# Kernel tuning notes

Hardware: AMD Instinct MI355X
Metric: run time of the kernel (lower is better)

## Reference

```python
import jax, jax.numpy as jnp
import numpy as np
from jax import lax

B, C, H, W = 2, 384, 32, 32
N_HEAD, N_GROUP = 12, 6
HC = C // N_HEAD          # 32 head channels
GC = C // N_GROUP         # 64 group channels
GH = N_HEAD // N_GROUP    # 2 heads per group
KK = 7                    # depthwise kernel (25<=32<=48)
OFF_FACTOR = 2.0
SCALE = HC ** -0.5
EPS = 1e-5


def setup_inputs() -> dict:
    key = jax.random.key(0)
    ks = jax.random.split(key, 16)
    s = 0.02
    inp = {
        "x": jax.random.normal(ks[0], (B, C, H, W), jnp.float32),
        "Wq": jax.random.normal(ks[1], (C, C), jnp.float32) * s,
        "bq": jnp.zeros((C,), jnp.float32),
        "Wk": jax.random.normal(ks[2], (C, C), jnp.float32) * s,
        "bk": jnp.zeros((C,), jnp.float32),
        "Wv": jax.random.normal(ks[3], (C, C), jnp.float32) * s,
        "bv": jnp.zeros((C,), jnp.float32),
        "Wo": jax.random.normal(ks[4], (C, C), jnp.float32) * s,
        "bo": jnp.zeros((C,), jnp.float32),
        "off_dw_w": jax.random.normal(ks[5], (GC, 1, KK, KK), jnp.float32) * s,  # depthwise OIHW
        "off_dw_b": jnp.zeros((GC,), jnp.float32),
        "ln_g": jnp.ones((GC,), jnp.float32),
        "ln_b": jnp.zeros((GC,), jnp.float32),
        "off_pw_w": jax.random.normal(ks[6], (2, GC), jnp.float32) * s,  # 1x1 conv, no bias
        "rpe_table": jax.random.normal(ks[7], (N_HEAD, 2 * H - 1, 2 * W - 1), jnp.float32) * 0.01,
    }
    return inp


def _ref_points(Hk, Wk):
    # torch.linspace(0.5, Hk-0.5, Hk)/Hk*2-1 == ((i+0.5)/Hk)*2-1
    ry = ((jnp.arange(Hk, dtype=jnp.float32) + 0.5) / Hk) * 2.0 - 1.0
    rx = ((jnp.arange(Wk, dtype=jnp.float32) + 0.5) / Wk) * 2.0 - 1.0
    gy, gx = jnp.meshgrid(ry, rx, indexing='ij')
    return jnp.stack((gy, gx), axis=-1)  # [Hk, Wk, 2] in (y, x) order


def _grid_sample(img, grid):
    # img: [N, Cc, Hi, Wi]; grid: [N, Hg, Wg, 2] in (x, y), align_corners=True, zeros padding
    N, Cc, Hi, Wi = img.shape
    Hg, Wg = grid.shape[1], grid.shape[2]
    gx = (grid[..., 0] + 1.0) * 0.5 * (Wi - 1)
    gy = (grid[..., 1] + 1.0) * 0.5 * (Hi - 1)
    x0 = jnp.floor(gx)
    y0 = jnp.floor(gy)
    wx = gx - x0
    wy = gy - y0
    img_f = img.reshape(N, Cc, Hi * Wi)

    def corner(xi, yi, w):
        valid = (xi >= 0) & (xi <= Wi - 1) & (yi >= 0) & (yi <= Hi - 1)
        xc = jnp.clip(xi, 0, Wi - 1).astype(jnp.int32)
        yc = jnp.clip(yi, 0, Hi - 1).astype(jnp.int32)
        idx = (yc * Wi + xc).reshape(N, 1, Hg * Wg)
        vals = jnp.take_along_axis(img_f, jnp.broadcast_to(idx, (N, Cc, Hg * Wg)), axis=2)
        w = (w * valid.astype(img.dtype)).reshape(N, 1, Hg * Wg)
        return vals * w

    out = (corner(x0, y0, (1 - wx) * (1 - wy))
           + corner(x0 + 1, y0, wx * (1 - wy))
           + corner(x0, y0 + 1, (1 - wx) * wy)
           + corner(x0 + 1, y0 + 1, wx * wy))
    return out.reshape(N, Cc, Hg, Wg)


def _conv1x1(x, w, b=None):
    y = jnp.einsum('bchw,oc->bohw', x, w)
    if b is not None:
        y = y + b[None, :, None, None]
    return y


def _forward(x, Wq, bq, Wk, bk, Wv, bv, Wo, bo, off_dw_w, off_dw_b, ln_g, ln_b, off_pw_w, rpe_table):
    q = _conv1x1(x, Wq, bq)                                        # [B, C, H, W]
    q_off = q.reshape(B * N_GROUP, GC, H, W)
    # conv_offset: depthwise conv -> LayerNorm(ch) -> GELU -> 1x1 conv to 2 ch
    o = lax.conv_general_dilated(q_off, off_dw_w, (1, 1), ((KK // 2, KK // 2), (KK // 2, KK // 2)),
                                 feature_group_count=GC,
                                 dimension_numbers=('NCHW', 'OIHW', 'NCHW'))
    o = o + off_dw_b[None, :, None, None]
    mu = jnp.mean(o, axis=1, keepdims=True)
    var = jnp.mean((o - mu) ** 2, axis=1, keepdims=True)
    o = (o - mu) * lax.rsqrt(var + EPS) * ln_g[None, :, None, None] + ln_b[None, :, None, None]
    o = jax.nn.gelu(o, approximate=False)
    off = jnp.einsum('bchw,oc->bohw', o, off_pw_w)                 # [BG, 2, Hs, Ws]
    Hs, Ws = off.shape[2], off.shape[3]
    n_sample = Hs * Ws
    off_range = jnp.array([1.0 / Hs, 1.0 / Ws], jnp.float32).reshape(1, 2, 1, 1)
    off = jnp.tanh(off) * off_range * OFF_FACTOR
    off = jnp.transpose(off, (0, 2, 3, 1))                         # [BG, Hs, Ws, 2] (y, x)
    pos = off + _ref_points(Hs, Ws)[None]                          # [BG, Hs, Ws, 2]

    x_g = x.reshape(B * N_GROUP, GC, H, W)
    x_s = _grid_sample(x_g, pos[..., ::-1])                        # [BG, GC, Hs, Ws]
    x_s = x_s.reshape(B, C, 1, n_sample)

    k = _conv1x1(x_s, Wk, bk).reshape(B * N_HEAD, HC, n_sample)
    v = _conv1x1(x_s, Wv, bv).reshape(B * N_HEAD, HC, n_sample)
    qh = q.reshape(B * N_HEAD, HC, H * W)
    attn = jnp.einsum('bcm,bcn->bmn', qh, k) * SCALE               # [BH, HW, ns]

    # RPE: bilinear lookup of relative-position table at query-sample displacements
    q_grid = _ref_points(H, W).reshape(1, H * W, 1, 2)
    disp = (q_grid - pos.reshape(B * N_GROUP, 1, n_sample, 2)) * 0.5  # [BG, HW, ns, 2] (y, x)
    rpe_b = jnp.broadcast_to(rpe_table[None], (B, N_HEAD, 2 * H - 1, 2 * W - 1))
    rpe_b = rpe_b.reshape(B * N_GROUP, GH, 2 * H - 1, 2 * W - 1)
    attn_bias = _grid_sample(rpe_b, disp[..., ::-1])               # [BG, GH, HW, ns]
    attn = attn + attn_bias.reshape(B * N_HEAD, H * W, n_sample)

    attn = jax.nn.softmax(attn, axis=2)
    out = jnp.einsum('bmn,bcn->bcm', attn, v).reshape(B, C, H, W)
    y = _conv1x1(out, Wo, bo)
    return y


def reference(x, Wq, bq, Wk, bk, Wv, bv, Wo, bo, off_dw_w, off_dw_b, ln_g, ln_b, off_pw_w, rpe_table):
    return _forward(x, Wq, bq, Wk, bk, Wv, bv, Wo, bo,
                    off_dw_w, off_dw_b, ln_g, ln_b, off_pw_w, rpe_table)
```

## Files before the change

### kernel.cpp

```cpp
#include <hip/hip_runtime.h>
#include <hip/hip_fp16.h>
#include <math.h>

#define HH 32
#define WW 32
#define HWSZ 1024
#define CC 384
#define NHEAD 12
#define NGROUP 6
#define HC 32
#define GC 64
#define NS 1024
#define ATTN_SCALE 0.17677669529663687f

typedef _Float16 half8_t __attribute__((ext_vector_type(8)));
typedef _Float16 half4_t __attribute__((ext_vector_type(4)));
typedef _Float16 half2_t __attribute__((ext_vector_type(2)));
typedef float    f4_t    __attribute__((ext_vector_type(4)));

template<int XLO>
__global__ __launch_bounds__(256) void gemm_wx(
    const float* __restrict__ W, const float* __restrict__ bias,
    const float* __restrict__ X, float* __restrict__ Y)
{
    const int bz = blockIdx.z;
    const int tm = blockIdx.y * 32;
    const int tn = blockIdx.x * 64;
    const int tid = threadIdx.x;
    const int w = tid >> 6, lane = tid & 63;
    const int quad = lane >> 4, lcol = lane & 15;

    __shared__ _Float16 sWh[32][40];
    __shared__ _Float16 sXh[64][40];
    __shared__ _Float16 sXl[XLO ? 64 : 1][40];

    const float* Xb = X + (size_t)bz * CC * 1024;
    float* Yb = Y + (size_t)bz * CC * 1024;

    f4_t acc0 = {0.f, 0.f, 0.f, 0.f}, acc1 = {0.f, 0.f, 0.f, 0.f};

    for (int k0 = 0; k0 < CC; k0 += 32) {
        {
            int m = tid >> 3, k4 = (tid & 7) * 4;
            float4 wv = *(const float4*)&W[(size_t)(tm + m) * CC + k0 + k4];
            half4_t h; h[0] = (_Float16)wv.x; h[1] = (_Float16)wv.y;
            h[2] = (_Float16)wv.z; h[3] = (_Float16)wv.w;
            *(half4_t*)&sWh[m][k4] = h;
        }
        {
            int k = tid >> 3, nj = tid & 7;
            const float* xr = &Xb[(size_t)(k0 + k) * 1024 + tn + nj];
#pragma unroll
            for (int i = 0; i < 8; ++i) {
                float v = xr[8 * i];
                _Float16 h = (_Float16)v;
                sXh[nj + 8 * i][k] = h;
                if (XLO) sXl[nj + 8 * i][k] = (_Float16)(v - (float)h);
            }
        }
        __syncthreads();

        half8_t Ah0 = *(const half8_t*)&sWh[lcol][quad * 8];
        half8_t Ah1 = *(const half8_t*)&sWh[16 + lcol][quad * 8];
        half8_t Bh  = *(const half8_t*)&sXh[w * 16 + lcol][quad * 8];
        acc0 = __builtin_amdgcn_mfma_f32_16x16x32_f16(Ah0, Bh, acc0, 0, 0, 0);
        acc1 = __builtin_amdgcn_mfma_f32_16x16x32_f16(Ah1, Bh, acc1, 0, 0, 0);
        if (XLO) {
            half8_t Bl = *(const half8_t*)&sXl[w * 16 + lcol][quad * 8];
            acc0 = __builtin_amdgcn_mfma_f32_16x16x32_f16(Ah0, Bl, acc0, 0, 0, 0);
            acc1 = __builtin_amdgcn_mfma_f32_16x16x32_f16(Ah1, Bl, acc1, 0, 0, 0);
        }
        __syncthreads();
    }

#pragma unroll
    for (int r = 0; r < 4; ++r) {
        int m0 = tm + quad * 4 + r;
        Yb[(size_t)m0 * 1024 + tn + w * 16 + lcol]        = acc0[r] + bias[m0];
        Yb[(size_t)(m0 + 16) * 1024 + tn + w * 16 + lcol] = acc1[r] + bias[m0 + 16];
    }
}

__global__ __launch_bounds__(256) void gemm_kv_fused(
    const float* __restrict__ Wk, const float* __restrict__ bk,
    const float* __restrict__ Wv, const float* __restrict__ bv,
    const float* __restrict__ X,
    _Float16* __restrict__ khT, _Float16* __restrict__ vhb)
{
    const int bz = blockIdx.z;
    const int head = blockIdx.y;
    const int tm = head * 32;
    const int tn = blockIdx.x * 64;
    const int tid = threadIdx.x;
    const int w = tid >> 6, lane = tid & 63;
    const int quad = lane >> 4, lcol = lane & 15;
    const int bh = bz * 12 + head;

    __shared__ _Float16 sWk[32][40], sWv[32][40];
    __shared__ _Float16 sXh[64][40];

    const float* Xb = X + (size_t)bz * CC * 1024;

    f4_t ak0 = {0.f, 0.f, 0.f, 0.f}, ak1 = {0.f, 0.f, 0.f, 0.f};
    f4_t av0 = {0.f, 0.f, 0.f, 0.f}, av1 = {0.f, 0.f, 0.f, 0.f};

    for (int k0 = 0; k0 < CC; k0 += 32) {
        {
            int m = tid >> 3, k4 = (tid & 7) * 4;
            float4 wk = *(const float4*)&Wk[(size_t)(tm + m) * CC + k0 + k4];
            float4 wv = *(const float4*)&Wv[(size_t)(tm + m) * CC + k0 + k4];
            half4_t hk; hk[0] = (_Float16)wk.x; hk[1] = (_Float16)wk.y;
            hk[2] = (_Float16)wk.z; hk[3] = (_Float16)wk.w;
            half4_t hv; hv[0] = (_Float16)wv.x; hv[1] = (_Float16)wv.y;
            hv[2] = (_Float16)wv.z; hv[3] = (_Float16)wv.w;
            *(half4_t*)&sWk[m][k4] = hk;
            *(half4_t*)&sWv[m][k4] = hv;
        }
        {
            int k = tid >> 3, nj = tid & 7;
            const float* xr = &Xb[(size_t)(k0 + k) * 1024 + tn + nj];
#pragma unroll
            for (int i = 0; i < 8; ++i)
                sXh[nj + 8 * i][k] = (_Float16)xr[8 * i];
        }
        __syncthreads();

        half8_t Xa = *(const half8_t*)&sXh[w * 16 + lcol][quad * 8];
        half8_t K0 = *(const half8_t*)&sWk[lcol][quad * 8];
        half8_t K1 = *(const half8_t*)&sWk[16 + lcol][quad * 8];
        half8_t V0 = *(const half8_t*)&sWv[lcol][quad * 8];
        half8_t V1 = *(const half8_t*)&sWv[16 + lcol][quad * 8];
        ak0 = __builtin_amdgcn_mfma_f32_16x16x32_f16(Xa, K0, ak0, 0, 0, 0);
        ak1 = __builtin_amdgcn_mfma_f32_16x16x32_f16(Xa, K1, ak1, 0, 0, 0);
        av0 = __builtin_amdgcn_mfma_f32_16x16x32_f16(V0, Xa, av0, 0, 0, 0);
        av1 = __builtin_amdgcn_mfma_f32_16x16x32_f16(V1, Xa, av1, 0, 0, 0);
        __syncthreads();
    }

    {
        float bk0 = bk[tm + lcol], bk1 = bk[tm + 16 + lcol];
#pragma unroll
        for (int r = 0; r < 4; ++r) {
            int n = tn + w * 16 + quad * 4 + r;
            khT[((size_t)bh * 1024 + n) * 32 + lcol]      = (_Float16)(ak0[r] + bk0);
            khT[((size_t)bh * 1024 + n) * 32 + 16 + lcol] = (_Float16)(ak1[r] + bk1);
        }
    }
    {
#pragma unroll
        for (int r = 0; r < 4; ++r) {
            int hc0 = quad * 4 + r;
            vhb[((size_t)bh * 32 + hc0) * 1024 + tn + w * 16 + lcol] =
                (_Float16)(av0[r] + bv[tm + hc0]);
            vhb[((size_t)bh * 32 + hc0 + 16) * 1024 + tn + w * 16 + lcol] =
                (_Float16)(av1[r] + bv[tm + hc0 + 16]);
        }
    }
}

__global__ __launch_bounds__(256) void dwconv_kernel(
    const float* __restrict__ q, const float* __restrict__ dww,
    const float* __restrict__ dwb, float* __restrict__ oconv)
{
    const int bc = blockIdx.x;
    const int bg = bc >> 6, c = bc & 63;
    const int b = bg / 6, g = bg % 6;
    const float* plane = q + ((size_t)b * CC + g * 64 + c) * 1024;

    __shared__ float sp[1024];
    __shared__ float sw[49];
    const int tid = threadIdx.x;
    for (int i = tid; i < 1024; i += 256) sp[i] = plane[i];
    if (tid < 49) sw[tid] = dww[c * 49 + tid];
    __syncthreads();

    const float bias = dwb[c];
    for (int i = tid; i < 1024; i += 256) {
        int y = i >> 5, x = i & 31;
        float s = 0.f;
#pragma unroll
        for (int ky = 0; ky < 7; ++ky) {
            int yy = y + ky - 3;
            if (yy < 0 || yy > 31) continue;
#pragma unroll
            for (int kx = 0; kx < 7; ++kx) {
                int xx = x + kx - 3;
                if (xx < 0 || xx > 31) continue;
                s += sp[yy * 32 + xx] * sw[ky * 7 + kx];
            }
        }
        oconv[(size_t)bc * 1024 + i] = s + bias;
    }
}

__global__ __launch_bounds__(256) void offset_sample_kernel(
    const float* __restrict__ oconv, const float* __restrict__ lng,
    const float* __restrict__ lnb, const float* __restrict__ pw,
    const float* __restrict__ x, float* __restrict__ pos,
    float* __restrict__ xs)
{
    const int bg = blockIdx.y;
    const int cs = blockIdx.z;
    const int px0 = blockIdx.x * 64;
    const int t = threadIdx.x;
    const int cg = t >> 6, pl = t & 63;
    const int px = px0 + pl;
    const int b = bg / 6, g = bg % 6;

    __shared__ float red[4][64];
    __shared__ float spos[64][2];

    const float* base = oconv + ((size_t)bg * 64 + cg * 16) * 1024 + px;
    float col[16];
    float s = 0.f;
#pragma unroll
    for (int i = 0; i < 16; ++i) { col[i] = base[(size_t)i * 1024]; s += col[i]; }
    red[cg][pl] = s;
    __syncthreads();
    float mu = (red[0][pl] + red[1][pl] + red[2][pl] + red[3][pl]) * (1.f / 64.f);
    float v = 0.f;
#pragma unroll
    for (int i = 0; i < 16; ++i) { float d = col[i] - mu; v += d * d; }
    __syncthreads();
    red[cg][pl] = v;
    __syncthreads();
    float inv = rsqrtf((red[0][pl] + red[1][pl] + red[2][pl] + red[3][pl]) * (1.f / 64.f) + 1e-5f);

    float oy = 0.f, ox = 0.f;
#pragma unroll
    for (int i = 0; i < 16; ++i) {
        int c = cg * 16 + i;
        float val = (col[i] - mu) * inv * lng[c] + lnb[c];
        float gl = 0.5f * val * (1.f + erff(val * 0.70710678118654752440f));
        oy += gl * pw[c];
        ox += gl * pw[64 + c];
    }
    __syncthreads();
    red[cg][pl] = oy;
    __syncthreads();
    float oyt = red[0][pl] + red[1][pl] + red[2][pl] + red[3][pl];
    __syncthreads();
    red[cg][pl] = ox;
    __syncthreads();
    if (cg == 0) {
        float oxt = red[0][pl] + red[1][pl] + red[2][pl] + red[3][pl];
        float offy = tanhf(oyt) * (2.0f / 32.0f);
        float offx = tanhf(oxt) * (2.0f / 32.0f);
        int y = px >> 5, xx = px & 31;
        float ry = ((y + 0.5f) / 32.f) * 2.f - 1.f;
        float rx = ((xx + 0.5f) / 32.f) * 2.f - 1.f;
        float py = offy + ry, pxv = offx + rx;
        spos[pl][0] = py; spos[pl][1] = pxv;
        if (cs == 0) {
            pos[((size_t)bg * 1024 + px) * 2 + 0] = py;
            pos[((size_t)bg * 1024 + px) * 2 + 1] = pxv;
        }
    }
    __syncthreads();

    float py = spos[pl][0], pxv = spos[pl][1];
    float gx = (pxv + 1.f) * 0.5f * 31.f;
    float gy = (py + 1.f) * 0.5f * 31.f;
    float x0f = floorf(gx), y0f = floorf(gy);
    float wx = gx - x0f, wy = gy - y0f;
    int x0 = (int)x0f, y0 = (int)y0f;
    float vx0 = ((unsigned)x0 <= 31u) ? 1.f : 0.f;
    float vx1 = ((unsigned)(x0 + 1) <= 31u) ? 1.f : 0.f;
    float vy0 = ((unsigned)y0 <= 31u) ? 1.f : 0.f;
    float vy1 = ((unsigned)(y0 + 1) <= 31u) ? 1.f : 0.f;
    float w00 = (1.f - wx) * (1.f - wy) * vx0 * vy0;
    float w01 = wx * (1.f - wy) * vx1 * vy0;
    float w10 = (1.f - wx) * wy * vx0 * vy1;
    float w11 = wx * wy * vx1 * vy1;
    int xc0 = min(max(x0, 0), 31), xc1 = min(max(x0 + 1, 0), 31);
    int yc0 = min(max(y0, 0), 31), yc1 = min(max(y0 + 1, 0), 31);
    int i00 = yc0 * 32 + xc0, i01 = yc0 * 32 + xc1;
    int i10 = yc1 * 32 + xc0, i11 = yc1 * 32 + xc1;

    const int c0 = cs * 16 + cg * 4;
    const float* xb = x + ((size_t)b * CC + g * 64 + c0) * 1024;
    float* xso = xs + ((size_t)b * CC + g * 64 + c0) * 1024 + px;
#pragma unroll
    for (int i = 0; i < 4; ++i) {
        const float* plane = xb + (size_t)i * 1024;
        xso[(size_t)i * 1024] = plane[i00] * w00 + plane[i01] * w01
                              + plane[i10] * w10 + plane[i11] * w11;
    }
}

__global__ __launch_bounds__(256) void attn_mfma_kernel(
    const float* __restrict__ q, const _Float16* __restrict__ khT,
    const _Float16* __restrict__ vhb, const float* __restrict__ pos,
    const float* __restrict__ rpe, float* __restrict__ out)
{
    const int bgp = blockIdx.y;
    const int b = bgp / 6, g = bgp % 6;
    const int h0 = g * 2;
    const int bh0 = b * 12 + h0, bh1 = bh0 + 1;
    const int mblk = blockIdx.x * 16;
    const int tid = threadIdx.x;
    const int w = tid >> 6, lane = tid & 63;
    const int quad = lane >> 4, lcol = lane & 15;

    __shared__ __align__(16) char smem[50944];
    half2_t*  srpeA = (half2_t*)smem;
    half2_t*  srpeB = (half2_t*)(smem + 8832);
    _Float16* sqh   = (_Float16*)(smem + 17664);
    _Float16* spw   = (_Float16*)(smem + 19712) + w * 2304;
    float*    cml0  = (float*)(smem + 38144);
    float*    cml1  = (float*)(smem + 38400);
    float2*   skxy  = (float2*)(smem + 38656);
    int*      siy   = (int*)(smem + 46848);
    float*    comb0 = (float*)(smem + 19712);
    float*    comb1 = (float*)(smem + 19712 + 9216);

    const float qyw = (((mblk >> 5) + 0.5f) * (1.f / 32.f)) * 2.f - 1.f;
    int r0; {
        float gy_lo = (qyw - 1.03125f) * 15.5f + 31.f;
        r0 = (int)floorf(gy_lo);
        r0 = min(max(r0, 0), 28);
    }

    {
        const float* rp0 = rpe + (size_t)h0 * 3969;
        const float* rp1 = rp0 + 3969;
        for (int i = tid; i < 35 * 63; i += 256) {
            int y = i / 63, xx = i - y * 63;
            int gi = (r0 + y) * 63 + xx;
            float a0 = rp0[gi], b0 = (xx < 62) ? rp0[gi + 1] : 0.f;
            float a1 = rp1[gi], b1 = (xx < 62) ? rp1[gi + 1] : 0.f;
            half2_t hA; hA[0] = (_Float16)a0; hA[1] = (_Float16)a1;
            half2_t hB; hB[0] = (_Float16)b0; hB[1] = (_Float16)b1;
            srpeA[i] = hA;
            srpeB[i] = hB;
        }
    }
    {
        const float* qb = q + ((size_t)b * CC + h0 * 32) * 1024 + mblk;
        for (int i = tid; i < 1024; i += 256) {
            int hh = i >> 9, rem = i & 511;
            int hc = rem >> 4, m = rem & 15;
            sqh[hh * 512 + m * 32 + hc] =
                (_Float16)qb[(size_t)(hh * 32 + hc) * 1024 + m];
        }
    }
    {
        const float2* pgv = (const float2*)(pos + (size_t)bgp * 2048);
        for (int i = tid; i < 1024; i += 256) {
            float2 pp = pgv[i];
            float gy = (qyw - pp.x) * 15.5f + 31.f;
            float y0f = floorf(gy);
            skxy[i] = make_float2(pp.y, gy - y0f);
            siy[i] = ((int)y0f - r0) * 63;
        }
    }
    __syncthreads();

    half8_t qf0 = *(const half8_t*)&sqh[lcol * 32 + quad * 8];
    half8_t qf1 = *(const half8_t*)&sqh[512 + lcol * 32 + quad * 8];
    const float qx = (((mblk & 31) + lcol + 0.5f) * (1.f / 32.f)) * 2.f - 1.f;

    const _Float16* khb0 = khT + (size_t)bh0 * 1024 * 32;
    const _Float16* khb1 = khT + (size_t)bh1 * 1024 * 32;
    const _Float16* vhh0 = vhb + (size_t)bh0 * 32 * 1024;
    const _Float16* vhh1 = vhb + (size_t)bh1 * 32 * 1024;

    f4_t o00 = {0.f, 0.f, 0.f, 0.f}, o01 = {0.f, 0.f, 0.f, 0.f};
    f4_t o10 = {0.f, 0.f, 0.f, 0.f}, o11 = {0.f, 0.f, 0.f, 0.f};
    float lsum0 = 0.f, lsum1 = 0.f;

#pragma unroll 1
    for (int c = 0; c < 4; ++c) {
        const int n0 = w * 256 + c * 64;

        half8_t khv0[4], khv1[4];
#pragma unroll
        for (int t = 0; t < 4; ++t) {
            size_t off = (size_t)(n0 + t * 16 + lcol) * 32 + quad * 8;
            khv0[t] = *(const half8_t*)&khb0[off];
            khv1[t] = *(const half8_t*)&khb1[off];
        }

        f4_t S0[4], S1[4];
#pragma unroll
        for (int t = 0; t < 4; ++t) {
            f4_t s0 = {0.f, 0.f, 0.f, 0.f}, s1 = {0.f, 0.f, 0.f, 0.f};
            s0 = __builtin_amdgcn_mfma_f32_16x16x32_f16(khv0[t], qf0, s0, 0, 0, 0);
            s1 = __builtin_amdgcn_mfma_f32_16x16x32_f16(khv1[t], qf1, s1, 0, 0, 0);
#pragma unroll
            for (int r = 0; r < 4; ++r) {
                int key = n0 + t * 16 + quad * 4 + r;
                float2 kxy = skxy[key];
                int iy = siy[key];
                float gx = (qx - kxy.x) * 15.5f + 31.f;
                float x0f = floorf(gx);
                float wxf = gx - x0f;
                int i00 = iy + (int)x0f;
                half2_t a0 = srpeA[i00];
                half2_t b0 = srpeB[i00];
                half2_t a1 = srpeA[i00 + 63];
                half2_t b1 = srpeB[i00 + 63];
                _Float16 wxs = (_Float16)wxf;
                _Float16 wys = (_Float16)kxy.y;
                half2_t wxh; wxh[0] = wxs; wxh[1] = wxs;
                half2_t wyh; wyh[0] = wys; wyh[1] = wys;
                half2_t top = a0 + (b0 - a0) * wxh;
                half2_t bot = a1 + (b1 - a1) * wxh;
                half2_t res = top + (bot - top) * wyh;
                s0[r] = s0[r] * ATTN_SCALE + (float)res[0];
                s1[r] = s1[r] * ATTN_SCALE + (float)res[1];
            }
            S0[t] = s0; S1[t] = s1;
        }

        half8_t vv00[2], vv01[2];
#pragma unroll
        for (int kp = 0; kp < 2; ++kp) {
            int nb = n0 + kp * 32 + quad * 8;
            vv00[kp] = *(const half8_t*)&vhh0[(size_t)lcol * 1024 + nb];
            vv01[kp] = *(const half8_t*)&vhh0[(size_t)(16 + lcol) * 1024 + nb];
        }

#pragma unroll
        for (int t = 0; t < 4; ++t) {
            float p0 = __expf(S0[t][0]), p1 = __expf(S0[t][1]);
            float p2 = __expf(S0[t][2]), p3 = __expf(S0[t][3]);
            lsum0 += (p0 + p1) + (p2 + p3);
            half4_t h;
            h[0] = (_Float16)p0; h[1] = (_Float16)p1;
            h[2] = (_Float16)p2; h[3] = (_Float16)p3;
            *(half4_t*)&spw[lcol * 72 + t * 16 + quad * 4] = h;
            float r0e = __expf(S1[t][0]), r1e = __expf(S1[t][1]);
            float r2e = __expf(S1[t][2]), r3e = __expf(S1[t][3]);
            lsum1 += (r0e + r1e) + (r2e + r3e);
            half4_t h1;
            h1[0] = (_Float16)r0e; h1[1] = (_Float16)r1e;
            h1[2] = (_Float16)r2e; h1[3] = (_Float16)r3e;
            *(half4_t*)&spw[1152 + lcol * 72 + t * 16 + quad * 4] = h1;
        }

#pragma unroll
        for (int kp = 0; kp < 2; ++kp) {
            half8_t pb = *(const half8_t*)&spw[lcol * 72 + kp * 32 + quad * 8];
            o00 = __builtin_amdgcn_mfma_f32_16x16x32_f16(vv00[kp], pb, o00, 0, 0, 0);
            o01 = __builtin_amdgcn_mfma_f32_16x16x32_f16(vv01[kp], pb, o01, 0, 0, 0);
        }
#pragma unroll
        for (int kp = 0; kp < 2; ++kp) {
            int nb = n0 + kp * 32 + quad * 8;
            half8_t v0 = *(const half8_t*)&vhh1[(size_t)lcol * 1024 + nb];
            half8_t v1 = *(const half8_t*)&vhh1[(size_t)(16 + lcol) * 1024 + nb];
            half8_t pb = *(const half8_t*)&spw[1152 + lcol * 72 + kp * 32 + quad * 8];
            o10 = __builtin_amdgcn_mfma_f32_16x16x32_f16(v0, pb, o10, 0, 0, 0);
            o11 = __builtin_amdgcn_mfma_f32_16x16x32_f16(v1, pb, o11, 0, 0, 0);
        }
    }

    lsum0 += __shfl_xor(lsum0, 16); lsum0 += __shfl_xor(lsum0, 32);
    lsum1 += __shfl_xor(lsum1, 16); lsum1 += __shfl_xor(lsum1, 32);

    __syncthreads();

    *(f4_t*)&comb0[(w * 16 + lcol) * 36 + quad * 4]      = o00;
    *(f4_t*)&comb0[(w * 16 + lcol) * 36 + 16 + quad * 4] = o01;
    *(f4_t*)&comb1[(w * 16 + lcol) * 36 + quad * 4]      = o10;
    *(f4_t*)&comb1[(w * 16 + lcol) * 36 + 16 + quad * 4] = o11;
    if (quad == 0) {
        cml0[w * 16 + lcol] = lsum0;
        cml1[w * 16 + lcol] = lsum1;
    }
    __syncthreads();

#pragma unroll
    for (int i = 0; i < 2; ++i) {
        int idx = tid + i * 256;
        int qq = idx >> 5, hc = idx & 31;
        {
            float L = cml0[qq] + cml0[16 + qq] + cml0[32 + qq] + cml0[48 + qq];
            float o = comb0[(0 * 16 + qq) * 36 + hc]
                    + comb0[(1 * 16 + qq) * 36 + hc]
                    + comb0[(2 * 16 + qq) * 36 + hc]
                    + comb0[(3 * 16 + qq) * 36 + hc];
            out[((size_t)b * CC + h0 * 32 + hc) * 1024 + mblk + qq] = o / L;
        }
        {
            float L = cml1[qq] + cml1[16 + qq] + cml1[32 + qq] + cml1[48 + qq];
            float o = comb1[(0 * 16 + qq) * 36 + hc]
                    + comb1[(1 * 16 + qq) * 36 + hc]
                    + comb1[(2 * 16 + qq) * 36 + hc]
                    + comb1[(3 * 16 + qq) * 36 + hc];
            out[((size_t)b * CC + (h0 + 1) * 32 + hc) * 1024 + mblk + qq] = o / L;
        }
    }
}

extern "C" void kernel_launch(void* const* d_in, const int* in_sizes, int n_in,
                              void* d_out, int out_size, void* d_ws, size_t ws_size,
                              hipStream_t stream) {
    const float* x   = (const float*)d_in[0];
    const float* Wq  = (const float*)d_in[1];
    const float* bq  = (const float*)d_in[2];
    const float* Wk  = (const float*)d_in[3];
    const float* bk  = (const float*)d_in[4];
    const float* Wv  = (const float*)d_in[5];
    const float* bv  = (const float*)d_in[6];
    const float* Wo  = (const float*)d_in[7];
    const float* bo  = (const float*)d_in[8];
    const float* dww = (const float*)d_in[9];
    const float* dwb = (const float*)d_in[10];
    const float* lng = (const float*)d_in[11];
    const float* lnb = (const float*)d_in[12];
    const float* pw  = (const float*)d_in[13];
    const float* rpe = (const float*)d_in[14];

    float* ws = (float*)d_ws;
    const size_t SZ = 786432;
    float* qbuf  = ws;
    float* xs    = ws + 1 * SZ;
    float* abuf  = ws + 2 * SZ;
    float* oconv = ws + 3 * SZ;
    _Float16* khT = (_Float16*)(ws + 4 * SZ);
    _Float16* vhb = (_Float16*)(ws + 5 * SZ);
    float* pos   = ws + 6 * SZ;

    dim3 gqo(16, 12, 2);
    gemm_wx<0><<<gqo, 256, 0, stream>>>(Wq, bq, x, qbuf);
    dwconv_kernel<<<768, 256, 0, stream>>>(qbuf, dww, dwb, oconv);
    offset_sample_kernel<<<dim3(16, 12, 4), 256, 0, stream>>>(oconv, lng, lnb, pw, x, pos, xs);
    gemm_kv_fused<<<dim3(16, 12, 2), 256, 0, stream>>>(Wk, bk, Wv, bv, xs, khT, vhb);
    attn_mfma_kernel<<<dim3(64, 12), 256, 0, stream>>>(qbuf, khT, vhb, pos, rpe, abuf);
    gemm_wx<1><<<gqo, 256, 0, stream>>>(Wo, bo, abuf, (float*)d_out);
}
```

Baseline: 160.4 us.

## Fuse depthwise conv with offset/LN/sampling kernel and store sampled x in fp16

Merges the depthwise 7x7 conv and the LayerNorm/GELU/offset/bilinear-sampling kernel into one kernel per (row, batch-group). Each block stages the seven halo rows for all 64 channels in shared memory as fp16, which removes the oconv intermediate buffer and one launch. The sampled x tensor is now written in fp16, and the KV GEMM reads it with 8-wide vector loads, halving that traffic. In exchange the grid drops to 384 blocks, each heavier, and the conv inputs are rounded to fp16, which costs some precision.

Result: slower. 184.1 us (+14.8%).

```diff
diff --git a/kernel.cpp b/kernel.cpp
--- a/kernel.cpp
+++ b/kernel.cpp
@@ -84,7 +84,7 @@
 __global__ __launch_bounds__(256) void gemm_kv_fused(
     const float* __restrict__ Wk, const float* __restrict__ bk,
     const float* __restrict__ Wv, const float* __restrict__ bv,
-    const float* __restrict__ X,
+    const _Float16* __restrict__ X,
     _Float16* __restrict__ khT, _Float16* __restrict__ vhb)
 {
     const int bz = blockIdx.z;
@@ -99,7 +99,7 @@
     __shared__ _Float16 sWk[32][40], sWv[32][40];
     __shared__ _Float16 sXh[64][40];
 
-    const float* Xb = X + (size_t)bz * CC * 1024;
+    const _Float16* Xb = X + (size_t)bz * CC * 1024;
 
     f4_t ak0 = {0.f, 0.f, 0.f, 0.f}, ak1 = {0.f, 0.f, 0.f, 0.f};
     f4_t av0 = {0.f, 0.f, 0.f, 0.f}, av1 = {0.f, 0.f, 0.f, 0.f};
@@ -117,11 +117,11 @@
             *(half4_t*)&sWv[m][k4] = hv;
         }
         {
-            int k = tid >> 3, nj = tid & 7;
-            const float* xr = &Xb[(size_t)(k0 + k) * 1024 + tn + nj];
+            int k = tid >> 3, nj = (tid & 7) * 8;
+            half8_t hv = *(const half8_t*)&Xb[(size_t)(k0 + k) * 1024 + tn + nj];
 #pragma unroll
             for (int i = 0; i < 8; ++i)
-                sXh[nj + 8 * i][k] = (_Float16)xr[8 * i];
+                sXh[nj + i][k] = hv[i];
         }
         __syncthreads();
 
@@ -158,133 +158,168 @@
     }
 }
 
-__global__ __launch_bounds__(256) void dwconv_kernel(
+__global__ __launch_bounds__(256) void conv_offset_sample_kernel(
     const float* __restrict__ q, const float* __restrict__ dww,
-    const float* __restrict__ dwb, float* __restrict__ oconv)
-{
-    const int bc = blockIdx.x;
-    const int bg = bc >> 6, c = bc & 63;
-    const int b = bg / 6, g = bg % 6;
-    const float* plane = q + ((size_t)b * CC + g * 64 + c) * 1024;
-
-    __shared__ float sp[1024];
-    __shared__ float sw[49];
-    const int tid = threadIdx.x;
-    for (int i = tid; i < 1024; i += 256) sp[i] = plane[i];
-    if (tid < 49) sw[tid] = dww[c * 49 + tid];
-    __syncthreads();
-
-    const float bias = dwb[c];
-    for (int i = tid; i < 1024; i += 256) {
-        int y = i >> 5, x = i & 31;
-        float s = 0.f;
-#pragma unroll
-        for (int ky = 0; ky < 7; ++ky) {
-            int yy = y + ky - 3;
-            if (yy < 0 || yy > 31) continue;
-#pragma unroll
-            for (int kx = 0; kx < 7; ++kx) {
-                int xx = x + kx - 3;
-                if (xx < 0 || xx > 31) continue;
-                s += sp[yy * 32 + xx] * sw[ky * 7 + kx];
-            }
-        }
-        oconv[(size_t)bc * 1024 + i] = s + bias;
-    }
-}
-
-__global__ __launch_bounds__(256) void offset_sample_kernel(
-    const float* __restrict__ oconv, const float* __restrict__ lng,
+    const float* __restrict__ dwb, const float* __restrict__ lng,
     const float* __restrict__ lnb, const float* __restrict__ pw,
     const float* __restrict__ x, float* __restrict__ pos,
-    float* __restrict__ xs)
+    _Float16* __restrict__ xs)
 {
+    const int y  = blockIdx.x;
     const int bg = blockIdx.y;
-    const int cs = blockIdx.z;
-    const int px0 = blockIdx.x * 64;
-    const int t = threadIdx.x;
-    const int cg = t >> 6, pl = t & 63;
-    const int px = px0 + pl;
     const int b = bg / 6, g = bg % 6;
-
-    __shared__ float red[4][64];
-    __shared__ float spos[64][2];
-
-    const float* base = oconv + ((size_t)bg * 64 + cg * 16) * 1024 + px;
-    float col[16];
-    float s = 0.f;
-#pragma unroll
-    for (int i = 0; i < 16; ++i) { col[i] = base[(size_t)i * 1024]; s += col[i]; }
-    red[cg][pl] = s;
-    __syncthreads();
-    float mu = (red[0][pl] + red[1][pl] + red[2][pl] + red[3][pl]) * (1.f / 64.f);
-    float v = 0.f;
-#pragma unroll
-    for (int i = 0; i < 16; ++i) { float d = col[i] - mu; v += d * d; }
-    __syncthreads();
-    red[cg][pl] = v;
-    __syncthreads();
-    float inv = rsqrtf((red[0][pl] + red[1][pl] + red[2][pl] + red[3][pl]) * (1.f / 64.f) + 1e-5f);
-
-    float oy = 0.f, ox = 0.f;
-#pragma unroll
-    for (int i = 0; i < 16; ++i) {
-        int c = cg * 16 + i;
-        float val = (col[i] - mu) * inv * lng[c] + lnb[c];
-        float gl = 0.5f * val * (1.f + erff(val * 0.70710678118654752440f));
-        oy += gl * pw[c];
-        ox += gl * pw[64 + c];
-    }
-    __syncthreads();
-    red[cg][pl] = oy;
-    __syncthreads();
-    float oyt = red[0][pl] + red[1][pl] + red[2][pl] + red[3][pl];
-    __syncthreads();
-    red[cg][pl] = ox;
-    __syncthreads();
-    if (cg == 0) {
-        float oxt = red[0][pl] + red[1][pl] + red[2][pl] + red[3][pl];
-        float offy = tanhf(oyt) * (2.0f / 32.0f);
-        float offx = tanhf(oxt) * (2.0f / 32.0f);
-        int y = px >> 5, xx = px & 31;
-        float ry = ((y + 0.5f) / 32.f) * 2.f - 1.f;
-        float rx = ((xx + 0.5f) / 32.f) * 2.f - 1.f;
-        float py = offy + ry, pxv = offx + rx;
-        spos[pl][0] = py; spos[pl][1] = pxv;
-        if (cs == 0) {
-            pos[((size_t)bg * 1024 + px) * 2 + 0] = py;
-            pos[((size_t)bg * 1024 + px) * 2 + 1] = pxv;
-        }
-    }
-    __syncthreads();
-
-    float py = spos[pl][0], pxv = spos[pl][1];
-    float gx = (pxv + 1.f) * 0.5f * 31.f;
-    float gy = (py + 1.f) * 0.5f * 31.f;
-    float x0f = floorf(gx), y0f = floorf(gy);
-    float wx = gx - x0f, wy = gy - y0f;
-    int x0 = (int)x0f, y0 = (int)y0f;
-    float vx0 = ((unsigned)x0 <= 31u) ? 1.f : 0.f;
-    float vx1 = ((unsigned)(x0 + 1) <= 31u) ? 1.f : 0.f;
-    float vy0 = ((unsigned)y0 <= 31u) ? 1.f : 0.f;
-    float vy1 = ((unsigned)(y0 + 1) <= 31u) ? 1.f : 0.f;
-    float w00 = (1.f - wx) * (1.f - wy) * vx0 * vy0;
-    float w01 = wx * (1.f - wy) * vx1 * vy0;
-    float w10 = (1.f - wx) * wy * vx0 * vy1;
-    float w11 = wx * wy * vx1 * vy1;
-    int xc0 = min(max(x0, 0), 31), xc1 = min(max(x0 + 1, 0), 31);
-    int yc0 = min(max(y0, 0), 31), yc1 = min(max(y0 + 1, 0), 31);
-    int i00 = yc0 * 32 + xc0, i01 = yc0 * 32 + xc1;
-    int i10 = yc1 * 32 + xc0, i11 = yc1 * 32 + xc1;
-
-    const int c0 = cs * 16 + cg * 4;
-    const float* xb = x + ((size_t)b * CC + g * 64 + c0) * 1024;
-    float* xso = xs + ((size_t)b * CC + g * 64 + c0) * 1024 + px;
-#pragma unroll
-    for (int i = 0; i < 4; ++i) {
-        const float* plane = xb + (size_t)i * 1024;
-        xso[(size_t)i * 1024] = plane[i00] * w00 + plane[i01] * w01
-                              + plane[i10] * w10 + plane[i11] * w11;
+    const int tid = threadIdx.x;
+    const int cp = tid >> 3;
+    const int pq = tid & 7;
+    const int c0 = cp * 2, c1 = c0 + 1;
+
+    __shared__ _Float16 sq[64][7][39];
+    __shared__ _Float16 swh[64 * 49];
+    __shared__ float red[32][33];
+    __shared__ float muA[32], invA[32], tY[32];
+    __shared__ float spos[32][2];
+
+    const float* qb = q + ((size_t)b * CC + g * 64) * 1024;
+
+    for (int i = tid; i < 64 * 7 * 32; i += 256) {
+        int ch = i / 224;
+        int rem = i - ch * 224;
+        int ky = rem >> 5, col = rem & 31;
+        int row = y + ky - 3;
+        float v = ((unsigned)row <= 31u) ? qb[(size_t)ch * 1024 + row * 32 + col] : 0.f;
+        sq[ch][ky][col + 3] = (_Float16)v;
+    }
+    for (int i = tid; i < 64 * 7 * 6; i += 256) {
+        int ch = i / 42;
+        int rem = i - ch * 42;
+        int ky = rem / 6, j = rem - ky * 6;
+        sq[ch][ky][j < 3 ? j : j + 32] = (_Float16)0.f;
+    }
+    for (int i = tid; i < 64 * 49; i += 256)
+        swh[i] = (_Float16)dww[i];
+    __syncthreads();
+
+    float a0[4] = {0.f, 0.f, 0.f, 0.f}, a1[4] = {0.f, 0.f, 0.f, 0.f};
+#pragma unroll
+    for (int ky = 0; ky < 7; ++ky) {
+        const _Float16* r0 = &sq[c0][ky][pq * 4];
+        const _Float16* r1 = &sq[c1][ky][pq * 4];
+        float q0[10], q1[10];
+#pragma unroll
+        for (int j = 0; j < 10; ++j) { q0[j] = (float)r0[j]; q1[j] = (float)r1[j]; }
+#pragma unroll
+        for (int kx = 0; kx < 7; ++kx) {
+            float w0 = (float)swh[c0 * 49 + ky * 7 + kx];
+            float w1 = (float)swh[c1 * 49 + ky * 7 + kx];
+#pragma unroll
+            for (int p = 0; p < 4; ++p) {
+                a0[p] += q0[p + kx] * w0;
+                a1[p] += q1[p + kx] * w1;
+            }
+        }
+    }
+    {
+        float bb0 = dwb[c0], bb1 = dwb[c1];
+#pragma unroll
+        for (int p = 0; p < 4; ++p) { a0[p] += bb0; a1[p] += bb1; }
+    }
+
+#pragma unroll
+    for (int p = 0; p < 4; ++p) red[cp][pq * 4 + p] = a0[p] + a1[p];
+    __syncthreads();
+    if (tid < 32) {
+        float s = 0.f;
+        for (int j = 0; j < 32; ++j) s += red[j][tid];
+        muA[tid] = s * (1.f / 64.f);
+    }
+    __syncthreads();
+    float mu[4];
+#pragma unroll
+    for (int p = 0; p < 4; ++p) mu[p] = muA[pq * 4 + p];
+#pragma unroll
+    for (int p = 0; p < 4; ++p) {
+        float d0 = a0[p] - mu[p], d1 = a1[p] - mu[p];
+        red[cp][pq * 4 + p] = d0 * d0 + d1 * d1;
+    }
+    __syncthreads();
+    if (tid < 32) {
+        float s = 0.f;
+        for (int j = 0; j < 32; ++j) s += red[j][tid];
+        invA[tid] = rsqrtf(s * (1.f / 64.f) + 1e-5f);
+    }
+    __syncthreads();
+    float iv[4];
+#pragma unroll
+    for (int p = 0; p < 4; ++p) iv[p] = invA[pq * 4 + p];
+
+    float g0v = lng[c0], g1v = lng[c1], lb0 = lnb[c0], lb1 = lnb[c1];
+    float pwy0 = pw[c0], pwy1 = pw[c1], pwx0 = pw[64 + c0], pwx1 = pw[64 + c1];
+    float oyp[4], oxp[4];
+#pragma unroll
+    for (int p = 0; p < 4; ++p) {
+        float v0 = (a0[p] - mu[p]) * iv[p] * g0v + lb0;
+        float v1 = (a1[p] - mu[p]) * iv[p] * g1v + lb1;
+        float gl0 = 0.5f * v0 * (1.f + erff(v0 * 0.70710678118654752440f));
+        float gl1 = 0.5f * v1 * (1.f + erff(v1 * 0.70710678118654752440f));
+        oyp[p] = gl0 * pwy0 + gl1 * pwy1;
+        oxp[p] = gl0 * pwx0 + gl1 * pwx1;
+    }
+#pragma unroll
+    for (int p = 0; p < 4; ++p) red[cp][pq * 4 + p] = oyp[p];
+    __syncthreads();
+    if (tid < 32) {
+        float s = 0.f;
+        for (int j = 0; j < 32; ++j) s += red[j][tid];
+        tY[tid] = s;
+    }
+    __syncthreads();
+#pragma unroll
+    for (int p = 0; p < 4; ++p) red[cp][pq * 4 + p] = oxp[p];
+    __syncthreads();
+    if (tid < 32) {
+        float s = 0.f;
+        for (int j = 0; j < 32; ++j) s += red[j][tid];
+        float offy = tanhf(tY[tid]) * 0.0625f;
+        float offx = tanhf(s) * 0.0625f;
+        float ry = (y + 0.5f) * 0.0625f - 1.f;
+        float rx = (tid + 0.5f) * 0.0625f - 1.f;
+        float pyv = offy + ry, pxv = offx + rx;
+        spos[tid][0] = pyv; spos[tid][1] = pxv;
+        size_t gpx = (size_t)bg * 1024 + y * 32 + tid;
+        pos[gpx * 2 + 0] = pyv;
+        pos[gpx * 2 + 1] = pxv;
+    }
+    __syncthreads();
+
+    const float* xb0 = x + ((size_t)b * CC + g * 64 + c0) * 1024;
+    const float* xb1 = xb0 + 1024;
+    _Float16* xo0 = xs + ((size_t)b * CC + g * 64 + c0) * 1024 + y * 32;
+    _Float16* xo1 = xo0 + 1024;
+#pragma unroll
+    for (int p = 0; p < 4; ++p) {
+        int col = pq * 4 + p;
+        float pyv = spos[col][0], pxv = spos[col][1];
+        float gx = (pxv + 1.f) * 0.5f * 31.f;
+        float gy = (pyv + 1.f) * 0.5f * 31.f;
+        float x0f = floorf(gx), y0f = floorf(gy);
+        float wx = gx - x0f, wy = gy - y0f;
+        int x0 = (int)x0f, y0i = (int)y0f;
+        float vx0 = ((unsigned)x0 <= 31u) ? 1.f : 0.f;
+        float vx1 = ((unsigned)(x0 + 1) <= 31u) ? 1.f : 0.f;
+        float vy0 = ((unsigned)y0i <= 31u) ? 1.f : 0.f;
+        float vy1 = ((unsigned)(y0i + 1) <= 31u) ? 1.f : 0.f;
+        float w00 = (1.f - wx) * (1.f - wy) * vx0 * vy0;
+        float w01 = wx * (1.f - wy) * vx1 * vy0;
+        float w10 = (1.f - wx) * wy * vx0 * vy1;
+        float w11 = wx * wy * vx1 * vy1;
+        int xc0 = min(max(x0, 0), 31), xc1 = min(max(x0 + 1, 0), 31);
+        int yc0 = min(max(y0i, 0), 31), yc1 = min(max(y0i + 1, 0), 31);
+        int i00 = yc0 * 32 + xc0, i01 = yc0 * 32 + xc1;
+        int i10 = yc1 * 32 + xc0, i11 = yc1 * 32 + xc1;
+        float s0v = xb0[i00] * w00 + xb0[i01] * w01 + xb0[i10] * w10 + xb0[i11] * w11;
+        float s1v = xb1[i00] * w00 + xb1[i01] * w01 + xb1[i10] * w10 + xb1[i11] * w11;
+        xo0[col] = (_Float16)s0v;
+        xo1[col] = (_Float16)s1v;
     }
 }
 
@@ -516,17 +551,16 @@
     float* ws = (float*)d_ws;
     const size_t SZ = 786432;
     float* qbuf  = ws;
-    float* xs    = ws + 1 * SZ;
+    _Float16* xs = (_Float16*)(ws + 1 * SZ);
     float* abuf  = ws + 2 * SZ;
-    float* oconv = ws + 3 * SZ;
     _Float16* khT = (_Float16*)(ws + 4 * SZ);
     _Float16* vhb = (_Float16*)(ws + 5 * SZ);
     float* pos   = ws + 6 * SZ;
 
     dim3 gqo(16, 12, 2);
     gemm_wx<0><<<gqo, 256, 0, stream>>>(Wq, bq, x, qbuf);
-    dwconv_kernel<<<768, 256, 0, stream>>>(qbuf, dww, dwb, oconv);
-    offset_sample_kernel<<<dim3(16, 12, 4), 256, 0, stream>>>(oconv, lng, lnb, pw, x, pos, xs);
+    conv_offset_sample_kernel<<<dim3(32, 12), 256, 0, stream>>>(
+        qbuf, dww, dwb, lng, lnb, pw, x, pos, xs);
     gemm_kv_fused<<<dim3(16, 12, 2), 256, 0, stream>>>(Wk, bk, Wv, bv, xs, khT, vhb);
     attn_mfma_kernel<<<dim3(64, 12), 256, 0, stream>>>(qbuf, khT, vhb, pos, rpe, abuf);
     gemm_wx<1><<<gqo, 256, 0, stream>>>(Wo, bo, abuf, (float*)d_out);
```

## Split offset computation from sampling and store sampled features as fp16

Applied to the files above, without the earlier changes.

The fused offset+sample kernel previously recomputed the LayerNorm/GELU/offset projection in each of the 4 channel-split blocks. It is now split into a pos-only kernel that runs once per pixel group and a separate sampling kernel that reads pos from global memory. The sampled features xs are also written as fp16 so the KV GEMM can load them with vector half8 reads instead of strided float loads. The split adds a kernel launch and a global round trip for pos, and moves the fp16 rounding of the sampled values earlier in the pipeline.

Measured after the change: 163.3 us. Within noise of the previous version (+1.8%).

```diff
diff --git a/kernel.cpp b/kernel.cpp
--- a/kernel.cpp
+++ b/kernel.cpp
@@ -84,7 +84,7 @@
 __global__ __launch_bounds__(256) void gemm_kv_fused(
     const float* __restrict__ Wk, const float* __restrict__ bk,
     const float* __restrict__ Wv, const float* __restrict__ bv,
-    const float* __restrict__ X,
+    const _Float16* __restrict__ X,
     _Float16* __restrict__ khT, _Float16* __restrict__ vhb)
 {
     const int bz = blockIdx.z;
@@ -99,7 +99,7 @@
     __shared__ _Float16 sWk[32][40], sWv[32][40];
     __shared__ _Float16 sXh[64][40];
 
-    const float* Xb = X + (size_t)bz * CC * 1024;
+    const _Float16* Xb = X + (size_t)bz * CC * 1024;
 
     f4_t ak0 = {0.f, 0.f, 0.f, 0.f}, ak1 = {0.f, 0.f, 0.f, 0.f};
     f4_t av0 = {0.f, 0.f, 0.f, 0.f}, av1 = {0.f, 0.f, 0.f, 0.f};
@@ -117,11 +117,11 @@
             *(half4_t*)&sWv[m][k4] = hv;
         }
         {
-            int k = tid >> 3, nj = tid & 7;
-            const float* xr = &Xb[(size_t)(k0 + k) * 1024 + tn + nj];
+            int k = tid >> 3, nj = (tid & 7) * 8;
+            half8_t hv = *(const half8_t*)&Xb[(size_t)(k0 + k) * 1024 + tn + nj];
 #pragma unroll
             for (int i = 0; i < 8; ++i)
-                sXh[nj + 8 * i][k] = (_Float16)xr[8 * i];
+                sXh[nj + i][k] = hv[i];
         }
         __syncthreads();
 
@@ -193,11 +193,66 @@
     }
 }
 
-__global__ __launch_bounds__(256) void offset_sample_kernel(
+__global__ __launch_bounds__(256) void offset_pos_kernel(
     const float* __restrict__ oconv, const float* __restrict__ lng,
     const float* __restrict__ lnb, const float* __restrict__ pw,
-    const float* __restrict__ x, float* __restrict__ pos,
-    float* __restrict__ xs)
+    float* __restrict__ pos)
+{
+    const int bg = blockIdx.y;
+    const int px0 = blockIdx.x * 64;
+    const int t = threadIdx.x;
+    const int cg = t >> 6, pl = t & 63;
+    const int px = px0 + pl;
+
+    __shared__ float red[4][64];
+
+    const float* base = oconv + ((size_t)bg * 64 + cg * 16) * 1024 + px;
+    float col[16];
+    float s = 0.f;
+#pragma unroll
+    for (int i = 0; i < 16; ++i) { col[i] = base[(size_t)i * 1024]; s += col[i]; }
+    red[cg][pl] = s;
+    __syncthreads();
+    float mu = (red[0][pl] + red[1][pl] + red[2][pl] + red[3][pl]) * (1.f / 64.f);
+    float v = 0.f;
+#pragma unroll
+    for (int i = 0; i < 16; ++i) { float d = col[i] - mu; v += d * d; }
+    __syncthreads();
+    red[cg][pl] = v;
+    __syncthreads();
+    float inv = rsqrtf((red[0][pl] + red[1][pl] + red[2][pl] + red[3][pl]) * (1.f / 64.f) + 1e-5f);
+
+    float oy = 0.f, ox = 0.f;
+#pragma unroll
+    for (int i = 0; i < 16; ++i) {
+        int c = cg * 16 + i;
+        float val = (col[i] - mu) * inv * lng[c] + lnb[c];
+        float gl = 0.5f * val * (1.f + erff(val * 0.70710678118654752440f));
+        oy += gl * pw[c];
+        ox += gl * pw[64 + c];
+    }
+    __syncthreads();
+    red[cg][pl] = oy;
+    __syncthreads();
+    float oyt = red[0][pl] + red[1][pl] + red[2][pl] + red[3][pl];
+    __syncthreads();
+    red[cg][pl] = ox;
+    __syncthreads();
+    if (cg == 0) {
+        float oxt = red[0][pl] + red[1][pl] + red[2][pl] + red[3][pl];
+        float offy = tanhf(oyt) * (2.0f / 32.0f);
+        float offx = tanhf(oxt) * (2.0f / 32.0f);
+        int y = px >> 5, xx = px & 31;
+        float ry = ((y + 0.5f) / 32.f) * 2.f - 1.f;
+        float rx = ((xx + 0.5f) / 32.f) * 2.f - 1.f;
+        pos[((size_t)bg * 1024 + px) * 2 + 0] = offy + ry;
+        pos[((size_t)bg * 1024 + px) * 2 + 1] = offx + rx;
+    }
+}
+
+__global__ __launch_bounds__(256) void sample_kernel(
+    const float* __restrict__ pos, const float* __restrict__ x,
+    _Float16* __restrict__ xs)
 {
     const int bg = blockIdx.y;
     const int cs = blockIdx.z;
@@ -207,58 +262,8 @@
     const int px = px0 + pl;
     const int b = bg / 6, g = bg % 6;
 
-    __shared__ float red[4][64];
-    __shared__ float spos[64][2];
-
-    const float* base = oconv + ((size_t)bg * 64 + cg * 16) * 1024 + px;
-    float col[16];
-    float s = 0.f;
-#pragma unroll
-    for (int i = 0; i < 16; ++i) { col[i] = base[(size_t)i * 1024]; s += col[i]; }
-    red[cg][pl] = s;
-    __syncthreads();
-    float mu = (red[0][pl] + red[1][pl] + red[2][pl] + red[3][pl]) * (1.f / 64.f);
-    float v = 0.f;
-#pragma unroll
-    for (int i = 0; i < 16; ++i) { float d = col[i] - mu; v += d * d; }
-    __syncthreads();
-    red[cg][pl] = v;
-    __syncthreads();
-    float inv = rsqrtf((red[0][pl] + red[1][pl] + red[2][pl] + red[3][pl]) * (1.f / 64.f) + 1e-5f);
-
-    float oy = 0.f, ox = 0.f;
-#pragma unroll
-    for (int i = 0; i < 16; ++i) {
-        int c = cg * 16 + i;
-        float val = (col[i] - mu) * inv * lng[c] + lnb[c];
-        float gl = 0.5f * val * (1.f + erff(val * 0.70710678118654752440f));
-        oy += gl * pw[c];
-        ox += gl * pw[64 + c];
-    }
-    __syncthreads();
-    red[cg][pl] = oy;
-    __syncthreads();
-    float oyt = red[0][pl] + red[1][pl] + red[2][pl] + red[3][pl];
-    __syncthreads();
-    red[cg][pl] = ox;
-    __syncthreads();
-    if (cg == 0) {
-        float oxt = red[0][pl] + red[1][pl] + red[2][pl] + red[3][pl];
-        float offy = tanhf(oyt) * (2.0f / 32.0f);
-        float offx = tanhf(oxt) * (2.0f / 32.0f);
-        int y = px >> 5, xx = px & 31;
-        float ry = ((y + 0.5f) / 32.f) * 2.f - 1.f;
-        float rx = ((xx + 0.5f) / 32.f) * 2.f - 1.f;
-        float py = offy + ry, pxv = offx + rx;
-        spos[pl][0] = py; spos[pl][1] = pxv;
-        if (cs == 0) {
-            pos[((size_t)bg * 1024 + px) * 2 + 0] = py;
-            pos[((size_t)bg * 1024 + px) * 2 + 1] = pxv;
-        }
-    }
-    __syncthreads();
-
-    float py = spos[pl][0], pxv = spos[pl][1];
+    float2 pp = *(const float2*)&pos[((size_t)bg * 1024 + px) * 2];
+    float py = pp.x, pxv = pp.y;
     float gx = (pxv + 1.f) * 0.5f * 31.f;
     float gy = (py + 1.f) * 0.5f * 31.f;
     float x0f = floorf(gx), y0f = floorf(gy);
@@ -279,12 +284,12 @@
 
     const int c0 = cs * 16 + cg * 4;
     const float* xb = x + ((size_t)b * CC + g * 64 + c0) * 1024;
-    float* xso = xs + ((size_t)b * CC + g * 64 + c0) * 1024 + px;
+    _Float16* xso = xs + ((size_t)b * CC + g * 64 + c0) * 1024 + px;
 #pragma unroll
     for (int i = 0; i < 4; ++i) {
         const float* plane = xb + (size_t)i * 1024;
-        xso[(size_t)i * 1024] = plane[i00] * w00 + plane[i01] * w01
-                              + plane[i10] * w10 + plane[i11] * w11;
+        xso[(size_t)i * 1024] = (_Float16)(plane[i00] * w00 + plane[i01] * w01
+                                         + plane[i10] * w10 + plane[i11] * w11);
     }
 }
 
@@ -516,7 +521,7 @@
     float* ws = (float*)d_ws;
     const size_t SZ = 786432;
     float* qbuf  = ws;
-    float* xs    = ws + 1 * SZ;
+    _Float16* xs = (_Float16*)(ws + 1 * SZ);
     float* abuf  = ws + 2 * SZ;
     float* oconv = ws + 3 * SZ;
     _Float16* khT = (_Float16*)(ws + 4 * SZ);
@@ -526,7 +531,8 @@
     dim3 gqo(16, 12, 2);
     gemm_wx<0><<<gqo, 256, 0, stream>>>(Wq, bq, x, qbuf);
     dwconv_kernel<<<768, 256, 0, stream>>>(qbuf, dww, dwb, oconv);
-    offset_sample_kernel<<<dim3(16, 12, 4), 256, 0, stream>>>(oconv, lng, lnb, pw, x, pos, xs);
+    offset_pos_kernel<<<dim3(16, 12), 256, 0, stream>>>(oconv, lng, lnb, pw, pos);
+    sample_kernel<<<dim3(16, 12, 4), 256, 0, stream>>>(pos, x, xs);
     gemm_kv_fused<<<dim3(16, 12, 2), 256, 0, stream>>>(Wk, bk, Wv, bv, xs, khT, vhb);
     attn_mfma_kernel<<<dim3(64, 12), 256, 0, stream>>>(qbuf, khT, vhb, pos, rpe, abuf);
     gemm_wx<1><<<gqo, 256, 0, stream>>>(Wo, bo, abuf, (float*)d_out);
```
